# Optimization experiments

Measured on AMD Instinct MI355X. Metric: run time of the kernel, lower is better.

## Reference

```python
import jax, jax.numpy as jnp
import numpy as np

B, S, H, NH = 4, 2048, 2048, 16
HD = H // NH  # 128


def setup_inputs() -> dict:
    key = jax.random.key(0)
    ks = jax.random.split(key, 9)
    s = lambda fan_in: 1.0 / np.sqrt(fan_in)
    return {
        "hidden_state": jax.random.normal(ks[0], (B, S, H), dtype=jnp.float32),
        # Linear weights stored as [in, out]
        "w_q": jax.random.uniform(ks[1], (H, H), jnp.float32, -s(H), s(H)),
        "b_q": jax.random.uniform(ks[2], (H,), jnp.float32, -s(H), s(H)),
        "w_k": jax.random.uniform(ks[3], (H, HD), jnp.float32, -s(H), s(H)),
        "b_k": jax.random.uniform(ks[4], (HD,), jnp.float32, -s(H), s(H)),
        "w_v": jax.random.uniform(ks[5], (H, HD), jnp.float32, -s(H), s(H)),
        "b_v": jax.random.uniform(ks[6], (HD,), jnp.float32, -s(H), s(H)),
        "w_o": jax.random.uniform(ks[7], (H, H), jnp.float32, -s(H), s(H)),
        "b_o": jax.random.uniform(ks[8], (H,), jnp.float32, -s(H), s(H)),
    }


def reference(hidden_state, w_q, b_q, w_k, b_k, w_v, b_v, w_o, b_o):
    b = hidden_state.shape[0]
    q = hidden_state @ w_q + b_q                       # [B,S,H]
    k = hidden_state @ w_k + b_k                       # [B,S,HD] (single KV head)
    v = hidden_state @ w_v + b_v                       # [B,S,HD]
    q = q.reshape(b, -1, NH, HD).transpose(0, 2, 1, 3)  # [B,NH,S,HD]
    scale = jnp.sqrt(jnp.float32(HD))
    scores = jnp.einsum("bhqd,bkd->bhqk", q, k) / scale  # [B,NH,S,S]
    probs = jax.nn.softmax(scores, axis=-1)
    out = jnp.einsum("bhqk,bkd->bhqd", probs, v)        # [B,NH,S,HD]
    # Faithful to original: transpose(-1,-2) (NOT transpose(1,2)) then view
    out = jnp.swapaxes(out, -1, -2).reshape(b, -1, HD * NH)  # [B,S,H]
    return out @ w_o + b_o
```

## Files before the change

kernel.cpp:

```cpp
#include <hip/hip_runtime.h>
#include <math.h>


#define BATCH 4
#define SLEN 2048
#define HDIM 2048
#define NHEADS 16
#define HD 128

typedef __bf16 bf16x8 __attribute__((ext_vector_type(8)));
typedef float f32x4 __attribute__((ext_vector_type(4)));

__device__ __forceinline__ void gload_lds16(const void* g, void* l) {
    __builtin_amdgcn_global_load_lds(
        (const __attribute__((address_space(1))) void*)g,
        (__attribute__((address_space(3))) void*)l, 16, 0, 0);
}

__device__ __forceinline__ int xcd_swizzle(int bid, int nwg) {
    int cpx = nwg >> 3;
    return (bid & 7) * cpx + (bid >> 3);
}

__global__ void conv_bf16(const float* __restrict__ in, __bf16* __restrict__ out) {
    int i = (blockIdx.x * 256 + threadIdx.x) * 8;
    float4 a = *reinterpret_cast<const float4*>(in + i);
    float4 b = *reinterpret_cast<const float4*>(in + i + 4);
    bf16x8 o;
    o[0] = (__bf16)a.x; o[1] = (__bf16)a.y; o[2] = (__bf16)a.z; o[3] = (__bf16)a.w;
    o[4] = (__bf16)b.x; o[5] = (__bf16)b.y; o[6] = (__bf16)b.z; o[7] = (__bf16)b.w;
    *reinterpret_cast<bf16x8*>(out + i) = o;
}

__global__ void transpose_conv(const float* __restrict__ in, __bf16* __restrict__ out,
                               int R, int C) {
    __shared__ float tile[32][33];
    int c0 = blockIdx.x * 32, r0 = blockIdx.y * 32;
    int tr = threadIdx.x >> 5, tc = threadIdx.x & 31;
#pragma unroll
    for (int i = 0; i < 4; ++i)
        tile[tr + i * 8][tc] = in[(size_t)(r0 + tr + i * 8) * C + c0 + tc];
    __syncthreads();
#pragma unroll
    for (int i = 0; i < 4; ++i)
        out[(size_t)(c0 + tr + i * 8) * R + r0 + tc] = (__bf16)tile[tc][tr + i * 8];
}

template <int MODE>
__global__ __launch_bounds__(256) void gemm_bt(
    const __bf16* __restrict__ A, const __bf16* __restrict__ BT,
    const float* __restrict__ bias, void* __restrict__ Cout,
    int M, int N, int K, int nbx)
{
    __shared__ __bf16 As[128 * 64];
    __shared__ __bf16 Bs[128 * 64];
    const int t = threadIdx.x;
    const int lane = t & 63;
    const int w = t >> 6;
    const int wr = w >> 1, wc = w & 1;
    const int id = xcd_swizzle(blockIdx.x, gridDim.x);
    const int m0 = (id / nbx) << 7, n0 = (id % nbx) << 7;

    f32x4 acc[4][4] = {};
    const int l8 = (lane & 7) * 8;
    const int lr = lane >> 3;

    for (int k0 = 0; k0 < K; k0 += 64) {
        __syncthreads();
#pragma unroll
        for (int i = 0; i < 4; ++i) {
            int c = w * 4 + i;
            int row = c * 8 + lr;
            gload_lds16(A + (size_t)(m0 + row) * K + k0 + l8, (char*)As + c * 1024);
            gload_lds16(BT + (size_t)(n0 + row) * K + k0 + l8, (char*)Bs + c * 1024);
        }
        __syncthreads();
#pragma unroll
        for (int ks = 0; ks < 2; ++ks) {
            bf16x8 a[4], b[4];
#pragma unroll
            for (int i = 0; i < 4; ++i) {
                a[i] = *reinterpret_cast<const bf16x8*>(
                    As + (wr * 64 + i * 16 + (lane & 15)) * 64 + ks * 32 + (lane >> 4) * 8);
                b[i] = *reinterpret_cast<const bf16x8*>(
                    Bs + (wc * 64 + i * 16 + (lane & 15)) * 64 + ks * 32 + (lane >> 4) * 8);
            }
#pragma unroll
            for (int i = 0; i < 4; ++i)
#pragma unroll
                for (int j = 0; j < 4; ++j)
                    acc[i][j] = __builtin_amdgcn_mfma_f32_16x16x32_bf16(
                        a[i], b[j], acc[i][j], 0, 0, 0);
        }
    }

    const int col_l = lane & 15, rgrp = lane >> 4;
#pragma unroll
    for (int j = 0; j < 4; ++j) {
        int col = n0 + wc * 64 + j * 16 + col_l;
        float bv = bias[col];
#pragma unroll
        for (int i = 0; i < 4; ++i) {
            int rowb = m0 + wr * 64 + i * 16 + rgrp * 4;
#pragma unroll
            for (int r = 0; r < 4; ++r) {
                float v = acc[i][j][r] + bv;
                int row = rowb + r;
                if (MODE == 0)
                    ((float*)Cout)[(size_t)row * N + col] = v;
                else if (MODE == 1)
                    ((__bf16*)Cout)[(size_t)row * N + col] = (__bf16)v;
                else
                    ((__bf16*)Cout)[((size_t)(row >> 11) * HD + col) * SLEN
                                    + (row & (SLEN - 1))] = (__bf16)v;
            }
        }
    }
}

__attribute__((amdgpu_waves_per_eu(2, 4)))
__global__ __launch_bounds__(512) void mqa_attn_mfma(
    const __bf16* __restrict__ Q,
    const __bf16* __restrict__ K,
    const __bf16* __restrict__ VT,
    __bf16* __restrict__ T)
{
    __shared__ __align__(16) __bf16 smem[25600];
    __bf16* KsB = smem;
    __bf16* VtB = smem + 8192;
    __bf16 (*Ps)[16][72] = reinterpret_cast<__bf16(*)[16][72]>(smem + 16384);

    const int t = threadIdx.x;
    const int lane = t & 63;
    const int w = t >> 6;
    const int bid = xcd_swizzle(blockIdx.x, gridDim.x);
    const int qb = bid & 15;
    const int nh = (bid >> 4) & 15;
    const int b = bid >> 8;
    const int q0 = qb << 7;

    const int cl = lane & 15;
    const int rg = lane >> 4;

    bf16x8 qf[4];
    {
        const __bf16* qrow = Q + (size_t)(b * SLEN + q0 + w * 16 + cl) * HDIM
                             + nh * HD + rg * 8;
#pragma unroll
        for (int ks = 0; ks < 4; ++ks)
            qf[ks] = *reinterpret_cast<const bf16x8*>(qrow + ks * 32);
    }

    f32x4 O[8] = {};
    float m[4], l[4];
#pragma unroll
    for (int r = 0; r < 4; ++r) { m[r] = -__builtin_inff(); l[r] = 0.f; }

    const float scale = 0.08838834764831845f;

    const int k_row0 = (w * 2) * 4 + (lane >> 4);
    const int k_cc0  = lane & 15;
    const int v_row0 = (w * 2) * 8 + (lane >> 3);
    const int v_cc0  = lane & 7;

    for (int kk = 0; kk < SLEN; kk += 64) {
        __syncthreads();
#pragma unroll
        for (int j = 0; j < 2; ++j) {
            int idx = w * 2 + j;
            int row = k_row0 + j * 4;
            int cc  = k_cc0 ^ (row & 7);
            gload_lds16(K + (size_t)(b * SLEN + kk + row) * HD + cc * 8,
                        (char*)KsB + idx * 1024);
        }
#pragma unroll
        for (int j = 0; j < 2; ++j) {
            int idx = w * 2 + j;
            int row = v_row0 + j * 8;
            int cc  = v_cc0 ^ (row & 7);
            gload_lds16(VT + (size_t)(b * HD + row) * SLEN + kk + cc * 8,
                        (char*)VtB + idx * 1024);
        }
        __syncthreads();

        f32x4 s[4] = {};
#pragma unroll
        for (int cb = 0; cb < 4; ++cb) {
            const int row = cb * 16 + cl;
            const __bf16* kr = KsB + row * 128;
            const int sw = row & 7;
#pragma unroll
            for (int ks = 0; ks < 4; ++ks) {
                bf16x8 kf = *reinterpret_cast<const bf16x8*>(
                    kr + (((ks * 4 + rg) ^ sw) << 3));
                s[cb] = __builtin_amdgcn_mfma_f32_16x16x32_bf16(qf[ks], kf, s[cb], 0, 0, 0);
            }
        }

#pragma unroll
        for (int cb = 0; cb < 4; ++cb)
#pragma unroll
            for (int r = 0; r < 4; ++r) s[cb][r] *= scale;

        float rs[4];
#pragma unroll
        for (int r = 0; r < 4; ++r) {
            float tm = fmaxf(fmaxf(s[0][r], s[1][r]), fmaxf(s[2][r], s[3][r]));
            tm = fmaxf(tm, __shfl_xor(tm, 1));
            tm = fmaxf(tm, __shfl_xor(tm, 2));
            tm = fmaxf(tm, __shfl_xor(tm, 4));
            tm = fmaxf(tm, __shfl_xor(tm, 8));
            float mn = fmaxf(m[r], tm);
            float alpha = __expf(m[r] - mn);
            m[r] = mn;
            l[r] *= alpha;
#pragma unroll
            for (int dcb = 0; dcb < 8; ++dcb) O[dcb][r] *= alpha;
            rs[r] = 0.f;
        }
#pragma unroll
        for (int cb = 0; cb < 4; ++cb)
#pragma unroll
            for (int r = 0; r < 4; ++r) {
                float p = __expf(s[cb][r] - m[r]);
                rs[r] += p;
                Ps[w][rg * 4 + r][cb * 16 + cl] = (__bf16)p;
            }
#pragma unroll
        for (int r = 0; r < 4; ++r) {
            float v = rs[r];
            v += __shfl_xor(v, 1);
            v += __shfl_xor(v, 2);
            v += __shfl_xor(v, 4);
            v += __shfl_xor(v, 8);
            l[r] += v;
        }

        bf16x8 pf[2];
#pragma unroll
        for (int ks = 0; ks < 2; ++ks)
            pf[ks] = *reinterpret_cast<const bf16x8*>(&Ps[w][cl][ks * 32 + rg * 8]);
#pragma unroll
        for (int dcb = 0; dcb < 8; ++dcb) {
            const int row = dcb * 16 + cl;
            const __bf16* vr = VtB + row * 64;
            const int sw = row & 7;
#pragma unroll
            for (int ks = 0; ks < 2; ++ks) {
                bf16x8 vf = *reinterpret_cast<const bf16x8*>(
                    vr + (((ks * 4 + rg) ^ sw) << 3));
                O[dcb] = __builtin_amdgcn_mfma_f32_16x16x32_bf16(pf[ks], vf, O[dcb], 0, 0, 0);
            }
        }
    }

    __syncthreads();
    __bf16 (*Eb)[136] = reinterpret_cast<__bf16(*)[136]>(smem);
    float invl[4];
#pragma unroll
    for (int r = 0; r < 4; ++r) invl[r] = 1.0f / l[r];
#pragma unroll
    for (int dcb = 0; dcb < 8; ++dcb)
#pragma unroll
        for (int r = 0; r < 4; ++r)
            Eb[dcb * 16 + cl][w * 16 + rg * 4 + r] = (__bf16)(O[dcb][r] * invl[r]);
    __syncthreads();
#pragma unroll
    for (int i = 0; i < 4; ++i) {
        int id = i * 512 + t;
        int d = id >> 4, c = id & 15;
        float4 v = *reinterpret_cast<const float4*>(&Eb[d][c * 8]);
        *reinterpret_cast<float4*>(
            T + (size_t)(b * HDIM + nh * HD + d) * SLEN + q0 + c * 8) = v;
    }
}

extern "C" void kernel_launch(void* const* d_in, const int* in_sizes, int n_in,
                              void* d_out, int out_size, void* d_ws, size_t ws_size,
                              hipStream_t stream) {
    const float* hs  = (const float*)d_in[0];
    const float* w_q = (const float*)d_in[1];
    const float* b_q = (const float*)d_in[2];
    const float* w_k = (const float*)d_in[3];
    const float* b_k = (const float*)d_in[4];
    const float* w_v = (const float*)d_in[5];
    const float* b_v = (const float*)d_in[6];
    const float* w_o = (const float*)d_in[7];
    const float* b_o = (const float*)d_in[8];

    const int M = BATCH * SLEN;
    const size_t MH = (size_t)M * HDIM;

    __bf16* hs_b = (__bf16*)d_out;
    __bf16* Qb   = hs_b + MH;

    char* p = (char*)d_ws;
    __bf16* wqT = (__bf16*)p;             p += (size_t)HDIM * HDIM * 2;
    __bf16* woT = (__bf16*)p;             p += (size_t)HDIM * HDIM * 2;
    __bf16* wkT = (__bf16*)p;             p += (size_t)HD * HDIM * 2;
    __bf16* wvT = (__bf16*)p;             p += (size_t)HD * HDIM * 2;
    __bf16* Kb  = (__bf16*)p;             p += (size_t)M * HD * 2;
    __bf16* VTb = (__bf16*)p;             p += (size_t)M * HD * 2;
    __bf16* Tb  = (__bf16*)p;

    dim3 blk(256);

    conv_bf16<<<dim3(MH / (256 * 8)), blk, 0, stream>>>(hs, hs_b);
    transpose_conv<<<dim3(HDIM / 32, HDIM / 32), blk, 0, stream>>>(w_q, wqT, HDIM, HDIM);
    transpose_conv<<<dim3(HD / 32, HDIM / 32), blk, 0, stream>>>(w_k, wkT, HDIM, HD);
    transpose_conv<<<dim3(HD / 32, HDIM / 32), blk, 0, stream>>>(w_v, wvT, HDIM, HD);
    transpose_conv<<<dim3(HDIM / 32, HDIM / 32), blk, 0, stream>>>(w_o, woT, HDIM, HDIM);

    gemm_bt<1><<<dim3(16 * (M / 128)), blk, 0, stream>>>(
        hs_b, wqT, b_q, Qb, M, HDIM, HDIM, 16);
    gemm_bt<1><<<dim3(1 * (M / 128)), blk, 0, stream>>>(
        hs_b, wkT, b_k, Kb, M, HD, HDIM, 1);
    gemm_bt<2><<<dim3(1 * (M / 128)), blk, 0, stream>>>(
        hs_b, wvT, b_v, VTb, M, HD, HDIM, 1);

    mqa_attn_mfma<<<dim3(BATCH * NHEADS * (SLEN / 128)), dim3(512), 0, stream>>>(
        Qb, Kb, VTb, Tb);

    gemm_bt<0><<<dim3(16 * (M / 128)), blk, 0, stream>>>(
        Tb, woT, b_o, d_out, M, HDIM, HDIM, 16);
}
```

Measured before the change: 702.2 us.

## Double-buffer K/V in attention, lazily rescale softmax, and fuse K/V projections

The attention kernel now double-buffers the K and V^T tiles in LDS. The next tile's global-to-LDS loads are issued while the current tile is computed, which leaves one barrier per iteration. The softmax scale is folded into Q once at load time. The running-max rescale of O and l is skipped unless some row's max grows by more than 8, and the P scratch buffer uses an XOR swizzle. s_setprio is raised around the MFMA blocks. The separate K and V projection GEMMs are merged into one launch with N=256, relying on wkT and wvT being contiguous in the workspace. The costs are doubled LDS per block, which may limit occupancy, and extra bf16 rounding on the pre-scaled Q.

```diff
diff --git a/kernel.cpp b/kernel.cpp
--- a/kernel.cpp
+++ b/kernel.cpp
@@ -49,7 +49,8 @@
 template <int MODE>
 __global__ __launch_bounds__(256) void gemm_bt(
     const __bf16* __restrict__ A, const __bf16* __restrict__ BT,
-    const float* __restrict__ bias, void* __restrict__ Cout,
+    const float* __restrict__ bias, const float* __restrict__ bias2,
+    void* __restrict__ Cout, void* __restrict__ Cout2,
     int M, int N, int K, int nbx)
 {
     __shared__ __bf16 As[128 * 64];
@@ -98,7 +99,11 @@
 #pragma unroll
     for (int j = 0; j < 4; ++j) {
         int col = n0 + wc * 64 + j * 16 + col_l;
-        float bv = bias[col];
+        float bv;
+        if (MODE == 3)
+            bv = (col < HD) ? bias[col] : bias2[col - HD];
+        else
+            bv = bias[col];
 #pragma unroll
         for (int i = 0; i < 4; ++i) {
             int rowb = m0 + wr * 64 + i * 16 + rgrp * 4;
@@ -110,9 +115,13 @@
                     ((float*)Cout)[(size_t)row * N + col] = v;
                 else if (MODE == 1)
                     ((__bf16*)Cout)[(size_t)row * N + col] = (__bf16)v;
-                else
-                    ((__bf16*)Cout)[((size_t)(row >> 11) * HD + col) * SLEN
-                                    + (row & (SLEN - 1))] = (__bf16)v;
+                else {
+                    if (col < HD)
+                        ((__bf16*)Cout)[(size_t)row * HD + col] = (__bf16)v;
+                    else
+                        ((__bf16*)Cout2)[((size_t)(row >> 11) * HD + (col - HD)) * SLEN
+                                         + (row & (SLEN - 1))] = (__bf16)v;
+                }
             }
         }
     }
@@ -125,10 +134,10 @@
     const __bf16* __restrict__ VT,
     __bf16* __restrict__ T)
 {
-    __shared__ __align__(16) __bf16 smem[25600];
+    __shared__ __align__(16) __bf16 smem[40960];
     __bf16* KsB = smem;
-    __bf16* VtB = smem + 8192;
-    __bf16 (*Ps)[16][72] = reinterpret_cast<__bf16(*)[16][72]>(smem + 16384);
+    __bf16* VtB = smem + 16384;
+    __bf16* PsB = smem + 32768;
 
     const int t = threadIdx.x;
     const int lane = t & 63;
@@ -142,52 +151,69 @@
     const int cl = lane & 15;
     const int rg = lane >> 4;
 
+    const float scale = 0.08838834764831845f;
+
     bf16x8 qf[4];
     {
         const __bf16* qrow = Q + (size_t)(b * SLEN + q0 + w * 16 + cl) * HDIM
                              + nh * HD + rg * 8;
 #pragma unroll
-        for (int ks = 0; ks < 4; ++ks)
-            qf[ks] = *reinterpret_cast<const bf16x8*>(qrow + ks * 32);
+        for (int ks = 0; ks < 4; ++ks) {
+            bf16x8 raw = *reinterpret_cast<const bf16x8*>(qrow + ks * 32);
+#pragma unroll
+            for (int j = 0; j < 8; ++j)
+                qf[ks][j] = (__bf16)((float)raw[j] * scale);
+        }
     }
 
     f32x4 O[8] = {};
     float m[4], l[4];
 #pragma unroll
     for (int r = 0; r < 4; ++r) { m[r] = -__builtin_inff(); l[r] = 0.f; }
-
-    const float scale = 0.08838834764831845f;
 
     const int k_row0 = (w * 2) * 4 + (lane >> 4);
     const int k_cc0  = lane & 15;
     const int v_row0 = (w * 2) * 8 + (lane >> 3);
     const int v_cc0  = lane & 7;
 
-    for (int kk = 0; kk < SLEN; kk += 64) {
-        __syncthreads();
-#pragma unroll
-        for (int j = 0; j < 2; ++j) {
-            int idx = w * 2 + j;
-            int row = k_row0 + j * 4;
-            int cc  = k_cc0 ^ (row & 7);
-            gload_lds16(K + (size_t)(b * SLEN + kk + row) * HD + cc * 8,
-                        (char*)KsB + idx * 1024);
-        }
-#pragma unroll
-        for (int j = 0; j < 2; ++j) {
-            int idx = w * 2 + j;
-            int row = v_row0 + j * 8;
-            int cc  = v_cc0 ^ (row & 7);
-            gload_lds16(VT + (size_t)(b * HD + row) * SLEN + kk + cc * 8,
-                        (char*)VtB + idx * 1024);
-        }
-        __syncthreads();
+#define STAGE_KV(TILE, BUF)                                                     \
+    do {                                                                        \
+        int kk_ = (TILE) * 64;                                                  \
+        _Pragma("unroll")                                                       \
+        for (int j = 0; j < 2; ++j) {                                           \
+            int idx = w * 2 + j;                                                \
+            int row = k_row0 + j * 4;                                           \
+            int cc  = k_cc0 ^ (row & 7);                                        \
+            gload_lds16(K + (size_t)(b * SLEN + kk_ + row) * HD + cc * 8,       \
+                        (char*)(KsB + (BUF) * 8192) + idx * 1024);              \
+        }                                                                       \
+        _Pragma("unroll")                                                       \
+        for (int j = 0; j < 2; ++j) {                                           \
+            int idx = w * 2 + j;                                                \
+            int row = v_row0 + j * 8;                                           \
+            int cc  = v_cc0 ^ (row & 7);                                        \
+            gload_lds16(VT + (size_t)(b * HD + row) * SLEN + kk_ + cc * 8,      \
+                        (char*)(VtB + (BUF) * 8192) + idx * 1024);              \
+        }                                                                       \
+    } while (0)
+
+    STAGE_KV(0, 0);
+    __syncthreads();
+
+    int buf = 0;
+    const int NT = SLEN / 64;
+    for (int tt = 0; tt < NT; ++tt) {
+        if (tt + 1 < NT) STAGE_KV(tt + 1, buf ^ 1);
+
+        const __bf16* Kb_ = KsB + buf * 8192;
+        const __bf16* Vb_ = VtB + buf * 8192;
 
         f32x4 s[4] = {};
+        __builtin_amdgcn_s_setprio(1);
 #pragma unroll
         for (int cb = 0; cb < 4; ++cb) {
             const int row = cb * 16 + cl;
-            const __bf16* kr = KsB + row * 128;
+            const __bf16* kr = Kb_ + row * 128;
             const int sw = row & 7;
 #pragma unroll
             for (int ks = 0; ks < 4; ++ks) {
@@ -196,13 +222,9 @@
                 s[cb] = __builtin_amdgcn_mfma_f32_16x16x32_bf16(qf[ks], kf, s[cb], 0, 0, 0);
             }
         }
-
-#pragma unroll
-        for (int cb = 0; cb < 4; ++cb)
-#pragma unroll
-            for (int r = 0; r < 4; ++r) s[cb][r] *= scale;
-
-        float rs[4];
+        __builtin_amdgcn_s_setprio(0);
+
+        float tmax[4], mx = 0.f;
 #pragma unroll
         for (int r = 0; r < 4; ++r) {
             float tm = fmaxf(fmaxf(s[0][r], s[1][r]), fmaxf(s[2][r], s[3][r]));
@@ -210,21 +232,30 @@
             tm = fmaxf(tm, __shfl_xor(tm, 2));
             tm = fmaxf(tm, __shfl_xor(tm, 4));
             tm = fmaxf(tm, __shfl_xor(tm, 8));
-            float mn = fmaxf(m[r], tm);
-            float alpha = __expf(m[r] - mn);
-            m[r] = mn;
-            l[r] *= alpha;
-#pragma unroll
-            for (int dcb = 0; dcb < 8; ++dcb) O[dcb][r] *= alpha;
-            rs[r] = 0.f;
-        }
+            tmax[r] = tm;
+            mx = fmaxf(mx, tm - m[r]);
+        }
+        if (__any(mx > 8.f)) {
+#pragma unroll
+            for (int r = 0; r < 4; ++r) {
+                float mn = fmaxf(m[r], tmax[r]);
+                float alpha = __expf(m[r] - mn);
+                m[r] = mn;
+                l[r] *= alpha;
+#pragma unroll
+                for (int dcb = 0; dcb < 8; ++dcb) O[dcb][r] *= alpha;
+            }
+        }
+        float rs[4] = {0.f, 0.f, 0.f, 0.f};
 #pragma unroll
         for (int cb = 0; cb < 4; ++cb)
 #pragma unroll
             for (int r = 0; r < 4; ++r) {
                 float p = __expf(s[cb][r] - m[r]);
                 rs[r] += p;
-                Ps[w][rg * 4 + r][cb * 16 + cl] = (__bf16)p;
+                int row = rg * 4 + r;
+                int col = (cb * 16 + cl) ^ ((row & 7) << 3);
+                PsB[w * 1024 + row * 64 + col] = (__bf16)p;
             }
 #pragma unroll
         for (int r = 0; r < 4; ++r) {
@@ -239,11 +270,13 @@
         bf16x8 pf[2];
 #pragma unroll
         for (int ks = 0; ks < 2; ++ks)
-            pf[ks] = *reinterpret_cast<const bf16x8*>(&Ps[w][cl][ks * 32 + rg * 8]);
+            pf[ks] = *reinterpret_cast<const bf16x8*>(
+                PsB + w * 1024 + cl * 64 + (((ks * 4 + rg) ^ (cl & 7)) << 3));
+        __builtin_amdgcn_s_setprio(1);
 #pragma unroll
         for (int dcb = 0; dcb < 8; ++dcb) {
             const int row = dcb * 16 + cl;
-            const __bf16* vr = VtB + row * 64;
+            const __bf16* vr = Vb_ + row * 64;
             const int sw = row & 7;
 #pragma unroll
             for (int ks = 0; ks < 2; ++ks) {
@@ -252,9 +285,13 @@
                 O[dcb] = __builtin_amdgcn_mfma_f32_16x16x32_bf16(pf[ks], vf, O[dcb], 0, 0, 0);
             }
         }
-    }
-
-    __syncthreads();
+        __builtin_amdgcn_s_setprio(0);
+
+        __syncthreads();
+        buf ^= 1;
+    }
+#undef STAGE_KV
+
     __bf16 (*Eb)[136] = reinterpret_cast<__bf16(*)[136]>(smem);
     float invl[4];
 #pragma unroll
@@ -312,15 +349,13 @@
     transpose_conv<<<dim3(HDIM / 32, HDIM / 32), blk, 0, stream>>>(w_o, woT, HDIM, HDIM);
 
     gemm_bt<1><<<dim3(16 * (M / 128)), blk, 0, stream>>>(
-        hs_b, wqT, b_q, Qb, M, HDIM, HDIM, 16);
-    gemm_bt<1><<<dim3(1 * (M / 128)), blk, 0, stream>>>(
-        hs_b, wkT, b_k, Kb, M, HD, HDIM, 1);
-    gemm_bt<2><<<dim3(1 * (M / 128)), blk, 0, stream>>>(
-        hs_b, wvT, b_v, VTb, M, HD, HDIM, 1);
+        hs_b, wqT, b_q, nullptr, Qb, nullptr, M, HDIM, HDIM, 16);
+    gemm_bt<3><<<dim3(2 * (M / 128)), blk, 0, stream>>>(
+        hs_b, wkT, b_k, b_v, Kb, VTb, M, 2 * HD, HDIM, 2);
 
     mqa_attn_mfma<<<dim3(BATCH * NHEADS * (SLEN / 128)), dim3(512), 0, stream>>>(
         Qb, Kb, VTb, Tb);
 
     gemm_bt<0><<<dim3(16 * (M / 128)), blk, 0, stream>>>(
-        Tb, woT, b_o, d_out, M, HDIM, HDIM, 16);
-}
+        Tb, woT, b_o, nullptr, d_out, nullptr, M, HDIM, HDIM, 16);
+}
```

Result: faster. 644.0 us (-8.3%).
